# Kernel optimization log

Hardware: AMD Instinct MI355X
Metric: run time of the kernel (lower is better)

The kernel has to match this reference:

```python
import jax, jax.numpy as jnp
import numpy as np
from functools import partial

N = 8192      # nodes
E = 524288    # edges (before self-loops)
D = 64        # hidden dim (in_features == out_features)
L = 9         # conv layers: 1 start + (n_layers-2)=8 middle
MLP = 3       # depth_of_mlp


def setup_inputs() -> dict:
    key = jax.random.key(0)
    ks = jax.random.split(key, 12)
    s = 0.1  # weight scale
    return {
        "node_feat": jax.random.normal(ks[0], (N, 1), dtype=jnp.float32),
        "edge_src": jax.random.randint(ks[1], (E,), 0, N, dtype=jnp.int32),
        "edge_dst": jax.random.randint(ks[2], (E,), 0, N, dtype=jnp.int32),
        # stacked per-layer conv params (all layers operate at width D)
        "conv_W":  jax.random.normal(ks[3], (L, D, D), dtype=jnp.float32) * s,
        "conv_b":  jax.random.normal(ks[4], (L, D), dtype=jnp.float32) * s,
        "gru_Wih": jax.random.normal(ks[5], (L, 3 * D, D), dtype=jnp.float32) * s,
        "gru_Whh": jax.random.normal(ks[6], (L, 3 * D, D), dtype=jnp.float32) * s,
        "gru_bih": jax.random.normal(ks[7], (L, 3 * D), dtype=jnp.float32) * s,
        "gru_bhh": jax.random.normal(ks[8], (L, 3 * D), dtype=jnp.float32) * s,
        "mlp_W":   jax.random.normal(ks[9], (MLP, D, D), dtype=jnp.float32) * s,
        "mlp_b":   jax.random.normal(ks[10], (MLP, D), dtype=jnp.float32) * s,
    }


def _forward(node_feat, edge_src, edge_dst,
             conv_W, conv_b, gru_Wih, gru_Whh, gru_bih, gru_bhh,
             mlp_W, mlp_b):
    # dgl.add_self_loop
    loop = jnp.arange(N, dtype=edge_src.dtype)
    src = jnp.concatenate([edge_src, loop])
    dst = jnp.concatenate([edge_dst, loop])

    # GatedGraphConv pads feat with zeros up to out_feats
    h0 = jnp.pad(node_feat, ((0, 0), (0, D - node_feat.shape[1])))

    def conv_layer(h, params):
        W, b, Wih, Whh, bih, bhh = params
        hl = h @ W.T + b                                   # [N, D]
        # copy_u -> sum aggregation (gather from src, scatter-add to dst)
        a = jax.ops.segment_sum(hl[src], dst, num_segments=N)  # [N, D]
        # torch.nn.GRUCell (gate order: r, z, n)
        gi = a @ Wih.T + bih                               # [N, 3D]
        gh = h @ Whh.T + bhh                               # [N, 3D]
        i_r, i_z, i_n = jnp.split(gi, 3, axis=-1)
        h_r, h_z, h_n = jnp.split(gh, 3, axis=-1)
        r = jax.nn.sigmoid(i_r + h_r)
        z = jax.nn.sigmoid(i_z + h_z)
        n = jnp.tanh(i_n + r * h_n)
        h_new = (1.0 - z) * n + z * h
        return jax.nn.relu(h_new), None                    # F.relu after each conv

    h, _ = jax.lax.scan(conv_layer, h0,
                        (conv_W, conv_b, gru_Wih, gru_Whh, gru_bih, gru_bhh))

    # lastmlp: (Linear -> ReLU) x depth_of_mlp
    for i in range(MLP):
        h = jax.nn.relu(h @ mlp_W[i].T + mlp_b[i])

    edge_sim = h @ h.T                                     # [N, N]
    return edge_sim[None]                                  # [1, N, N]


def reference(node_feat, edge_src, edge_dst,
              conv_W, conv_b, gru_Wih, gru_Whh, gru_bih, gru_bhh,
              mlp_W, mlp_b):
    return _forward(node_feat, edge_src, edge_dst,
                    conv_W, conv_b, gru_Wih, gru_Whh, gru_bih, gru_bhh,
                    mlp_W, mlp_b)
```

## Files before the change

### kernel.cpp

```cpp
#include <hip/hip_runtime.h>
#include <math.h>

#define NNODES 8192
#define DDIM   64
#define NLAYER 9
#define NMLP   3

typedef short bfrag8 __attribute__((ext_vector_type(8)));
typedef float facc16 __attribute__((ext_vector_type(16)));

__global__ void prep_weights(const float* __restrict__ conv_W,
                             const float* __restrict__ gru_Whh,
                             const float* __restrict__ gru_Wih,
                             const float* __restrict__ mlp_W,
                             float* __restrict__ WtA,
                             float* __restrict__ WtI,
                             float* __restrict__ WtM)
{
    int tid = blockIdx.x * blockDim.x + threadIdx.x;
    const int nA = NLAYER * 64 * 256;
    const int nI = NLAYER * 64 * 192;
    const int nM = NMLP * 64 * 64;
    if (tid < nA) {
        int l = tid / 16384, rem = tid % 16384;
        int k = rem / 256, c = rem % 256;
        float v = (c < 64) ? conv_W[l * 4096 + c * 64 + k]
                           : gru_Whh[l * 12288 + (c - 64) * 64 + k];
        WtA[tid] = v;
    } else if (tid < nA + nI) {
        int t = tid - nA;
        int l = t / 12288, rem = t % 12288;
        int k = rem / 192, c = rem % 192;
        WtI[t] = gru_Wih[l * 12288 + c * 64 + k];
    } else if (tid < nA + nI + nM) {
        int t = tid - nA - nI;
        int m = t / 4096, rem = t % 4096;
        int k = rem / 64, c = rem % 64;
        WtM[t] = mlp_W[m * 4096 + c * 64 + k];
    }
}

__global__ void init_h(const float* __restrict__ node_feat,
                       float* __restrict__ h, int* __restrict__ counts)
{
    int tid = blockIdx.x * blockDim.x + threadIdx.x;
    if (tid < NNODES * DDIM) {
        int n = tid >> 6, d = tid & 63;
        h[tid] = (d == 0) ? node_feat[n] : 0.f;
    }
    if (tid < NNODES) counts[tid] = 0;
}

__global__ void count_deg(const int* __restrict__ dst, int E, int* __restrict__ counts)
{
    int tid = blockIdx.x * blockDim.x + threadIdx.x;
    if (tid < E) atomicAdd(&counts[dst[tid]], 1);
}

__global__ void scan_deg(const int* __restrict__ counts,
                         int* __restrict__ row_ptr, int* __restrict__ row_fill)
{
    __shared__ int partial[256];
    int t = threadIdx.x;
    int local[32];
    int base = t * 32;
    int s = 0;
    #pragma unroll
    for (int i = 0; i < 32; i++) { local[i] = counts[base + i]; s += local[i]; }
    partial[t] = s;
    __syncthreads();
    for (int off = 1; off < 256; off <<= 1) {
        int v = (t >= off) ? partial[t - off] : 0;
        __syncthreads();
        partial[t] += v;
        __syncthreads();
    }
    int run = (t == 0) ? 0 : partial[t - 1];
    #pragma unroll
    for (int i = 0; i < 32; i++) {
        row_ptr[base + i] = run;
        row_fill[base + i] = run;
        run += local[i];
    }
    if (t == 255) row_ptr[NNODES] = run;
}

__global__ void scatter_edges(const int* __restrict__ src, const int* __restrict__ dst, int E,
                              int* __restrict__ row_fill, int* __restrict__ col_idx)
{
    int tid = blockIdx.x * blockDim.x + threadIdx.x;
    if (tid < E) {
        int pos = atomicAdd(&row_fill[dst[tid]], 1);
        col_idx[pos] = src[tid];
    }
}

__global__ __launch_bounds__(256)
void layer_pre(const float* __restrict__ h,
               const float* __restrict__ Wt,
               const float* __restrict__ bA,
               const float* __restrict__ bH,
               float* __restrict__ hl, float* __restrict__ gh)
{
    __shared__ float ht[8][64];
    int c = threadIdx.x;
    int row0 = blockIdx.x * 8;
    ((float2*)ht)[c] = ((const float2*)(h + row0 * 64))[c];
    __syncthreads();
    float bias = (c < 64) ? bA[c] : bH[c - 64];
    float acc[8];
    #pragma unroll
    for (int r = 0; r < 8; r++) acc[r] = bias;
    #pragma unroll 8
    for (int k = 0; k < 64; k++) {
        float w = Wt[k * 256 + c];
        #pragma unroll
        for (int r = 0; r < 8; r++) acc[r] = fmaf(ht[r][k], w, acc[r]);
    }
    if (c < 64) {
        #pragma unroll
        for (int r = 0; r < 8; r++) hl[(row0 + r) * 64 + c] = acc[r];
    } else {
        int cc = c - 64;
        #pragma unroll
        for (int r = 0; r < 8; r++) gh[(row0 + r) * 192 + cc] = acc[r];
    }
}

__device__ __forceinline__ float sigmoidf_(float x) { return 1.f / (1.f + __expf(-x)); }
__device__ __forceinline__ float tanhf_(float x) {
    float e = __expf(-2.f * fabsf(x));
    float t = (1.f - e) / (1.f + e);
    return copysignf(t, x);
}

__global__ __launch_bounds__(256)
void layer_gru_agg(const float* __restrict__ hl,
                   const int* __restrict__ row_ptr,
                   const int* __restrict__ col_idx,
                   const float* __restrict__ WtI_l,
                   const float* __restrict__ bih,
                   const float* __restrict__ gh,
                   float* __restrict__ h)
{
    __shared__ float at[8][64];
    int tid = threadIdx.x;
    int d = tid & 63, rg = tid >> 6;
    int row0 = blockIdx.x * 8;
    #pragma unroll
    for (int s = 0; s < 2; s++) {
        int node = row0 + rg * 2 + s;
        int s0 = row_ptr[node], s1 = row_ptr[node + 1];
        float acc = hl[node * 64 + d];
        int e = s0;
        for (; e + 4 <= s1; e += 4) {
            int n0 = col_idx[e], n1 = col_idx[e + 1], n2 = col_idx[e + 2], n3 = col_idx[e + 3];
            float v0 = hl[n0 * 64 + d];
            float v1 = hl[n1 * 64 + d];
            float v2 = hl[n2 * 64 + d];
            float v3 = hl[n3 * 64 + d];
            acc += (v0 + v1) + (v2 + v3);
        }
        for (; e < s1; ++e)
            acc += hl[col_idx[e] * 64 + d];
        at[rg * 2 + s][d] = acc;
    }
    __syncthreads();
    float br = bih[d], bz = bih[64 + d], bn = bih[128 + d];
    float ar[2] = {br, br}, az[2] = {bz, bz}, an[2] = {bn, bn};
    #pragma unroll 8
    for (int k = 0; k < 64; k++) {
        float wr = WtI_l[k * 192 + d];
        float wz = WtI_l[k * 192 + 64 + d];
        float wn = WtI_l[k * 192 + 128 + d];
        #pragma unroll
        for (int s = 0; s < 2; s++) {
            float av = at[rg * 2 + s][k];
            ar[s] = fmaf(av, wr, ar[s]);
            az[s] = fmaf(av, wz, az[s]);
            an[s] = fmaf(av, wn, an[s]);
        }
    }
    #pragma unroll
    for (int s = 0; s < 2; s++) {
        int node = row0 + rg * 2 + s;
        float ghr = gh[node * 192 + d];
        float ghz = gh[node * 192 + 64 + d];
        float ghn = gh[node * 192 + 128 + d];
        float hv  = h[node * 64 + d];
        float r = sigmoidf_(ar[s] + ghr);
        float z = sigmoidf_(az[s] + ghz);
        float n = tanhf_(an[s] + r * ghn);
        float hn = (1.f - z) * n + z * hv;
        h[node * 64 + d] = fmaxf(hn, 0.f);
    }
}

__global__ __launch_bounds__(256)
void mlp_layer(const float* __restrict__ WtM_m,
               const float* __restrict__ b,
               float* __restrict__ h)
{
    __shared__ float ht[8][64];
    int tid = threadIdx.x;
    int d = tid & 63, rg = tid >> 6;
    int row0 = blockIdx.x * 8;
    ((float2*)ht)[tid] = ((const float2*)(h + row0 * 64))[tid];
    __syncthreads();
    float acc0 = b[d], acc1 = b[d];
    #pragma unroll 8
    for (int k = 0; k < 64; k++) {
        float w = WtM_m[k * 64 + d];
        acc0 = fmaf(ht[rg * 2 + 0][k], w, acc0);
        acc1 = fmaf(ht[rg * 2 + 1][k], w, acc1);
    }
    h[(row0 + rg * 2 + 0) * 64 + d] = fmaxf(acc0, 0.f);
    h[(row0 + rg * 2 + 1) * 64 + d] = fmaxf(acc1, 0.f);
}

__device__ __forceinline__ unsigned short f2bf_rne(float x) {
    unsigned int u = __float_as_uint(x);
    u += 0x7fffu + ((u >> 16) & 1u);
    return (unsigned short)(u >> 16);
}
__device__ __forceinline__ float bf2f(unsigned short b) {
    return __uint_as_float(((unsigned int)b) << 16);
}

__global__ __launch_bounds__(256)
void split_bf16(const float* __restrict__ h,
                unsigned short* __restrict__ h_hi,
                unsigned short* __restrict__ h_lo)
{
    int tid = blockIdx.x * blockDim.x + threadIdx.x;
    float x = h[tid];
    unsigned short hi = f2bf_rne(x);
    float r = x - bf2f(hi);
    h_hi[tid] = hi;
    h_lo[tid] = f2bf_rne(r);
}

__global__ __launch_bounds__(256)
void simmat_mfma(const unsigned short* __restrict__ h_hi,
                 const unsigned short* __restrict__ h_lo,
                 float* __restrict__ out)
{
    __shared__ uint4 smem[4096];
    int tid = threadIdx.x;
    int l = tid & 63, w = tid >> 6;
    int by = blockIdx.y, bx = blockIdx.x;

    #pragma unroll
    for (int q = 0; q < 8; q++) {
        int idx = tid + 256 * q;
        int row = idx >> 4, seg = idx & 15;
        const unsigned short* baseAB = (seg < 8) ? h_hi : h_lo;
        uint4 va = ((const uint4*)(baseAB + (by * 128 + row) * 64))[seg & 7];
        smem[row * 16 + (seg ^ (row & 15))] = va;
        uint4 vb = ((const uint4*)(baseAB + (bx * 128 + row) * 64))[seg & 7];
        smem[2048 + row * 16 + (seg ^ (row & 15))] = vb;
    }
    __syncthreads();

    int lr = l & 31, hi5 = l >> 5;
    facc16 acc[2][2];
    #pragma unroll
    for (int i = 0; i < 2; i++)
        #pragma unroll
        for (int j = 0; j < 2; j++) acc[i][j] = (facc16)(0.f);

    #pragma unroll
    for (int kk = 0; kk < 64; kk += 16) {
        int kq = (kk >> 3) + hi5;
        bfrag8 ahi[2], alo[2], bhi[2], blo[2];
        #pragma unroll
        for (int i = 0; i < 2; i++) {
            int arow = (w >> 1) * 64 + i * 32 + lr;
            ahi[i] = *(const bfrag8*)&smem[arow * 16 + (kq ^ (arow & 15))];
            alo[i] = *(const bfrag8*)&smem[arow * 16 + ((8 + kq) ^ (arow & 15))];
            int brow = (w & 1) * 64 + i * 32 + lr;
            bhi[i] = *(const bfrag8*)&smem[2048 + brow * 16 + (kq ^ (brow & 15))];
            blo[i] = *(const bfrag8*)&smem[2048 + brow * 16 + ((8 + kq) ^ (brow & 15))];
        }
        #pragma unroll
        for (int i = 0; i < 2; i++)
            #pragma unroll
            for (int j = 0; j < 2; j++) {
                acc[i][j] = __builtin_amdgcn_mfma_f32_32x32x16_bf16(ahi[i], bhi[j], acc[i][j], 0, 0, 0);
                acc[i][j] = __builtin_amdgcn_mfma_f32_32x32x16_bf16(ahi[i], blo[j], acc[i][j], 0, 0, 0);
                acc[i][j] = __builtin_amdgcn_mfma_f32_32x32x16_bf16(alo[i], bhi[j], acc[i][j], 0, 0, 0);
            }
    }

    int rbase = by * 128 + (w >> 1) * 64;
    int cbase = bx * 128 + (w & 1) * 64;
    int crow0 = rbase + 4 * hi5;
    int ccol0 = cbase + lr;
    #pragma unroll
    for (int i = 0; i < 2; i++)
        #pragma unroll
        for (int j = 0; j < 2; j++) {
            #pragma unroll
            for (int reg = 0; reg < 16; reg++) {
                int row = crow0 + i * 32 + (reg & 3) + 8 * (reg >> 2);
                int col = ccol0 + j * 32;
                out[(size_t)row * 8192 + col] = acc[i][j][reg];
            }
        }
}

extern "C" void kernel_launch(void* const* d_in, const int* in_sizes, int n_in,
                              void* d_out, int out_size, void* d_ws, size_t ws_size,
                              hipStream_t stream)
{
    const float* node_feat = (const float*)d_in[0];
    const int*   edge_src  = (const int*)d_in[1];
    const int*   edge_dst  = (const int*)d_in[2];
    const float* conv_W    = (const float*)d_in[3];
    const float* conv_b    = (const float*)d_in[4];
    const float* gru_Wih   = (const float*)d_in[5];
    const float* gru_Whh   = (const float*)d_in[6];
    const float* gru_bih   = (const float*)d_in[7];
    const float* gru_bhh   = (const float*)d_in[8];
    const float* mlp_W     = (const float*)d_in[9];
    const float* mlp_b     = (const float*)d_in[10];
    int E = in_sizes[1];
    float* out = (float*)d_out;

    float* ws  = (float*)d_ws;
    float* h   = ws;
    float* hl  = h  + NNODES * DDIM;
    float* gh  = hl + NNODES * DDIM;
    float* WtA = gh + NNODES * 192;
    float* WtI = WtA + NLAYER * 64 * 256;
    float* WtM = WtI + NLAYER * 64 * 192;
    int* counts   = (int*)(WtM + NMLP * 64 * 64);
    int* row_ptr  = counts + NNODES;
    int* row_fill = row_ptr + NNODES + 1;
    int* col_idx  = row_fill + NNODES;
    unsigned short* h_hi = (unsigned short*)((((uintptr_t)(col_idx + E)) + 15) & ~(uintptr_t)15);
    unsigned short* h_lo = h_hi + NNODES * DDIM;

    prep_weights<<<1056, 256, 0, stream>>>(conv_W, gru_Whh, gru_Wih, mlp_W, WtA, WtI, WtM);
    init_h<<<(NNODES * DDIM + 255) / 256, 256, 0, stream>>>(node_feat, h, counts);
    count_deg<<<(E + 255) / 256, 256, 0, stream>>>(edge_dst, E, counts);
    scan_deg<<<1, 256, 0, stream>>>(counts, row_ptr, row_fill);
    scatter_edges<<<(E + 255) / 256, 256, 0, stream>>>(edge_src, edge_dst, E, row_fill, col_idx);

    for (int l = 0; l < NLAYER; l++) {
        layer_pre<<<NNODES / 8, 256, 0, stream>>>(h, WtA + l * 16384,
                                                  conv_b + l * 64, gru_bhh + l * 192, hl, gh);
        layer_gru_agg<<<NNODES / 8, 256, 0, stream>>>(hl, row_ptr, col_idx,
                                                      WtI + l * 12288,
                                                      gru_bih + l * 192, gh, h);
    }
    for (int m = 0; m < NMLP; m++) {
        mlp_layer<<<NNODES / 8, 256, 0, stream>>>(WtM + m * 4096, mlp_b + m * 64, h);
    }
    split_bf16<<<NNODES * DDIM / 256, 256, 0, stream>>>(h, h_hi, h_lo);
    dim3 g(64, 64);
    simmat_mfma<<<g, 256, 0, stream>>>(h_hi, h_lo, out);
}
```

Baseline: 691.3 us.

## Aggregate raw h before conv linear and fuse each layer into one kernel

Uses linearity: the sum of (h W^T + b) over neighbours becomes (sum of h) W^T + deg*b, so the gather runs on the raw input h and the conv linear, the hidden-gate GEMM and the GRU all happen in one kernel per layer, with ping-pong h buffers. This removes the hl/gh intermediate round trips and halves the per-layer launches. It also merges the three MLP layers and the bf16 split into one kernel, and folds init/count into the weight-prep kernel with a memset. Per-block work grows (three small GEMMs per block), which may raise register pressure and lower occupancy, and the reordered summation changes floating-point rounding.

```diff
diff --git a/kernel.cpp b/kernel.cpp
--- a/kernel.cpp
+++ b/kernel.cpp
@@ -9,13 +9,17 @@
 typedef short bfrag8 __attribute__((ext_vector_type(8)));
 typedef float facc16 __attribute__((ext_vector_type(16)));
 
-__global__ void prep_weights(const float* __restrict__ conv_W,
-                             const float* __restrict__ gru_Whh,
-                             const float* __restrict__ gru_Wih,
-                             const float* __restrict__ mlp_W,
-                             float* __restrict__ WtA,
-                             float* __restrict__ WtI,
-                             float* __restrict__ WtM)
+__global__ void prep_all(const float* __restrict__ conv_W,
+                         const float* __restrict__ gru_Whh,
+                         const float* __restrict__ gru_Wih,
+                         const float* __restrict__ mlp_W,
+                         const float* __restrict__ node_feat,
+                         const int* __restrict__ edge_dst,
+                         float* __restrict__ WtA,
+                         float* __restrict__ WtI,
+                         float* __restrict__ WtM,
+                         float* __restrict__ h0,
+                         int* __restrict__ counts, int E)
 {
     int tid = blockIdx.x * blockDim.x + threadIdx.x;
     const int nA = NLAYER * 64 * 256;
@@ -24,9 +28,8 @@
     if (tid < nA) {
         int l = tid / 16384, rem = tid % 16384;
         int k = rem / 256, c = rem % 256;
-        float v = (c < 64) ? conv_W[l * 4096 + c * 64 + k]
-                           : gru_Whh[l * 12288 + (c - 64) * 64 + k];
-        WtA[tid] = v;
+        WtA[tid] = (c < 64) ? conv_W[l * 4096 + c * 64 + k]
+                            : gru_Whh[l * 12288 + (c - 64) * 64 + k];
     } else if (tid < nA + nI) {
         int t = tid - nA;
         int l = t / 12288, rem = t % 12288;
@@ -38,23 +41,11 @@
         int k = rem / 64, c = rem % 64;
         WtM[t] = mlp_W[m * 4096 + c * 64 + k];
     }
-}
-
-__global__ void init_h(const float* __restrict__ node_feat,
-                       float* __restrict__ h, int* __restrict__ counts)
-{
-    int tid = blockIdx.x * blockDim.x + threadIdx.x;
-    if (tid < NNODES * DDIM) {
+    {
         int n = tid >> 6, d = tid & 63;
-        h[tid] = (d == 0) ? node_feat[n] : 0.f;
-    }
-    if (tid < NNODES) counts[tid] = 0;
-}
-
-__global__ void count_deg(const int* __restrict__ dst, int E, int* __restrict__ counts)
-{
-    int tid = blockIdx.x * blockDim.x + threadIdx.x;
-    if (tid < E) atomicAdd(&counts[dst[tid]], 1);
+        h0[tid] = (d == 0) ? node_feat[n] : 0.f;
+    }
+    if (tid < E) atomicAdd(&counts[edge_dst[tid]], 1);
 }
 
 __global__ void scan_deg(const int* __restrict__ counts,
@@ -95,38 +86,6 @@
     }
 }
 
-__global__ __launch_bounds__(256)
-void layer_pre(const float* __restrict__ h,
-               const float* __restrict__ Wt,
-               const float* __restrict__ bA,
-               const float* __restrict__ bH,
-               float* __restrict__ hl, float* __restrict__ gh)
-{
-    __shared__ float ht[8][64];
-    int c = threadIdx.x;
-    int row0 = blockIdx.x * 8;
-    ((float2*)ht)[c] = ((const float2*)(h + row0 * 64))[c];
-    __syncthreads();
-    float bias = (c < 64) ? bA[c] : bH[c - 64];
-    float acc[8];
-    #pragma unroll
-    for (int r = 0; r < 8; r++) acc[r] = bias;
-    #pragma unroll 8
-    for (int k = 0; k < 64; k++) {
-        float w = Wt[k * 256 + c];
-        #pragma unroll
-        for (int r = 0; r < 8; r++) acc[r] = fmaf(ht[r][k], w, acc[r]);
-    }
-    if (c < 64) {
-        #pragma unroll
-        for (int r = 0; r < 8; r++) hl[(row0 + r) * 64 + c] = acc[r];
-    } else {
-        int cc = c - 64;
-        #pragma unroll
-        for (int r = 0; r < 8; r++) gh[(row0 + r) * 192 + cc] = acc[r];
-    }
-}
-
 __device__ __forceinline__ float sigmoidf_(float x) { return 1.f / (1.f + __expf(-x)); }
 __device__ __forceinline__ float tanhf_(float x) {
     float e = __expf(-2.f * fabsf(x));
@@ -135,87 +94,95 @@
 }
 
 __global__ __launch_bounds__(256)
-void layer_gru_agg(const float* __restrict__ hl,
-                   const int* __restrict__ row_ptr,
-                   const int* __restrict__ col_idx,
-                   const float* __restrict__ WtI_l,
-                   const float* __restrict__ bih,
-                   const float* __restrict__ gh,
-                   float* __restrict__ h)
-{
-    __shared__ float at[8][64];
+void layer_full(const float* __restrict__ hin,
+                const int* __restrict__ row_ptr,
+                const int* __restrict__ col_idx,
+                const float* __restrict__ WtA_l,
+                const float* __restrict__ WtI_l,
+                const float* __restrict__ cb,
+                const float* __restrict__ bih,
+                const float* __restrict__ bhh,
+                float* __restrict__ hout)
+{
+    __shared__ float hloc[8][64];
+    __shared__ float agg[8][64];
+    __shared__ float aLDS[8][64];
     int tid = threadIdx.x;
     int d = tid & 63, rg = tid >> 6;
     int row0 = blockIdx.x * 8;
+    ((float2*)hloc)[tid] = ((const float2*)(hin + row0 * 64))[tid];
     #pragma unroll
     for (int s = 0; s < 2; s++) {
         int node = row0 + rg * 2 + s;
         int s0 = row_ptr[node], s1 = row_ptr[node + 1];
-        float acc = hl[node * 64 + d];
+        float acc = hin[node * 64 + d];
         int e = s0;
         for (; e + 4 <= s1; e += 4) {
             int n0 = col_idx[e], n1 = col_idx[e + 1], n2 = col_idx[e + 2], n3 = col_idx[e + 3];
-            float v0 = hl[n0 * 64 + d];
-            float v1 = hl[n1 * 64 + d];
-            float v2 = hl[n2 * 64 + d];
-            float v3 = hl[n3 * 64 + d];
+            float v0 = hin[n0 * 64 + d];
+            float v1 = hin[n1 * 64 + d];
+            float v2 = hin[n2 * 64 + d];
+            float v3 = hin[n3 * 64 + d];
             acc += (v0 + v1) + (v2 + v3);
         }
         for (; e < s1; ++e)
-            acc += hl[col_idx[e] * 64 + d];
-        at[rg * 2 + s][d] = acc;
-    }
-    __syncthreads();
-    float br = bih[d], bz = bih[64 + d], bn = bih[128 + d];
-    float ar[2] = {br, br}, az[2] = {bz, bz}, an[2] = {bn, bn};
-    #pragma unroll 8
+            acc += hin[col_idx[e] * 64 + d];
+        agg[rg * 2 + s][d] = acc;
+    }
+    __syncthreads();
+    {
+        int r0 = rg * 2, r1 = rg * 2 + 1;
+        float deg0 = (float)(row_ptr[row0 + r0 + 1] - row_ptr[row0 + r0] + 1);
+        float deg1 = (float)(row_ptr[row0 + r1 + 1] - row_ptr[row0 + r1] + 1);
+        float cbd = cb[d];
+        float a0 = deg0 * cbd, a1 = deg1 * cbd;
+        #pragma unroll 8
+        for (int k = 0; k < 64; k++) {
+            float w = WtA_l[k * 256 + d];
+            a0 = fmaf(agg[r0][k], w, a0);
+            a1 = fmaf(agg[r1][k], w, a1);
+        }
+        aLDS[r0][d] = a0;
+        aLDS[r1][d] = a1;
+    }
+    __syncthreads();
+    float gir[2], giz[2], gin[2], ghr[2], ghz[2], ghn[2];
+    {
+        float br = bih[d], bz = bih[64 + d], bn = bih[128 + d];
+        float cr = bhh[d], cz = bhh[64 + d], cn = bhh[128 + d];
+        #pragma unroll
+        for (int s = 0; s < 2; s++) { gir[s]=br; giz[s]=bz; gin[s]=bn; ghr[s]=cr; ghz[s]=cz; ghn[s]=cn; }
+    }
+    #pragma unroll 4
     for (int k = 0; k < 64; k++) {
-        float wr = WtI_l[k * 192 + d];
-        float wz = WtI_l[k * 192 + 64 + d];
-        float wn = WtI_l[k * 192 + 128 + d];
+        float wir = WtI_l[k * 192 + d];
+        float wiz = WtI_l[k * 192 + 64 + d];
+        float win = WtI_l[k * 192 + 128 + d];
+        float whr = WtA_l[k * 256 + 64 + d];
+        float whz = WtA_l[k * 256 + 128 + d];
+        float whn = WtA_l[k * 256 + 192 + d];
         #pragma unroll
         for (int s = 0; s < 2; s++) {
-            float av = at[rg * 2 + s][k];
-            ar[s] = fmaf(av, wr, ar[s]);
-            az[s] = fmaf(av, wz, az[s]);
-            an[s] = fmaf(av, wn, an[s]);
+            float av = aLDS[rg * 2 + s][k];
+            float hv = hloc[rg * 2 + s][k];
+            gir[s] = fmaf(av, wir, gir[s]);
+            giz[s] = fmaf(av, wiz, giz[s]);
+            gin[s] = fmaf(av, win, gin[s]);
+            ghr[s] = fmaf(hv, whr, ghr[s]);
+            ghz[s] = fmaf(hv, whz, ghz[s]);
+            ghn[s] = fmaf(hv, whn, ghn[s]);
         }
     }
     #pragma unroll
     for (int s = 0; s < 2; s++) {
-        int node = row0 + rg * 2 + s;
-        float ghr = gh[node * 192 + d];
-        float ghz = gh[node * 192 + 64 + d];
-        float ghn = gh[node * 192 + 128 + d];
-        float hv  = h[node * 64 + d];
-        float r = sigmoidf_(ar[s] + ghr);
-        float z = sigmoidf_(az[s] + ghz);
-        float n = tanhf_(an[s] + r * ghn);
-        float hn = (1.f - z) * n + z * hv;
-        h[node * 64 + d] = fmaxf(hn, 0.f);
-    }
-}
-
-__global__ __launch_bounds__(256)
-void mlp_layer(const float* __restrict__ WtM_m,
-               const float* __restrict__ b,
-               float* __restrict__ h)
-{
-    __shared__ float ht[8][64];
-    int tid = threadIdx.x;
-    int d = tid & 63, rg = tid >> 6;
-    int row0 = blockIdx.x * 8;
-    ((float2*)ht)[tid] = ((const float2*)(h + row0 * 64))[tid];
-    __syncthreads();
-    float acc0 = b[d], acc1 = b[d];
-    #pragma unroll 8
-    for (int k = 0; k < 64; k++) {
-        float w = WtM_m[k * 64 + d];
-        acc0 = fmaf(ht[rg * 2 + 0][k], w, acc0);
-        acc1 = fmaf(ht[rg * 2 + 1][k], w, acc1);
-    }
-    h[(row0 + rg * 2 + 0) * 64 + d] = fmaxf(acc0, 0.f);
-    h[(row0 + rg * 2 + 1) * 64 + d] = fmaxf(acc1, 0.f);
+        int row = row0 + rg * 2 + s;
+        float r = sigmoidf_(gir[s] + ghr[s]);
+        float z = sigmoidf_(giz[s] + ghz[s]);
+        float n = tanhf_(gin[s] + r * ghn[s]);
+        float hv = hloc[rg * 2 + s][d];
+        float hnew = (1.f - z) * n + z * hv;
+        hout[row * 64 + d] = fmaxf(hnew, 0.f);
+    }
 }
 
 __device__ __forceinline__ unsigned short f2bf_rne(float x) {
@@ -228,16 +195,42 @@
 }
 
 __global__ __launch_bounds__(256)
-void split_bf16(const float* __restrict__ h,
-                unsigned short* __restrict__ h_hi,
-                unsigned short* __restrict__ h_lo)
-{
-    int tid = blockIdx.x * blockDim.x + threadIdx.x;
-    float x = h[tid];
-    unsigned short hi = f2bf_rne(x);
-    float r = x - bf2f(hi);
-    h_hi[tid] = hi;
-    h_lo[tid] = f2bf_rne(r);
+void mlp_split(const float* __restrict__ WtM,
+               const float* __restrict__ mlp_b,
+               const float* __restrict__ hin,
+               unsigned short* __restrict__ h_hi,
+               unsigned short* __restrict__ h_lo)
+{
+    __shared__ float buf0[8][64], buf1[8][64];
+    int tid = threadIdx.x, d = tid & 63, rg = tid >> 6;
+    int row0 = blockIdx.x * 8;
+    ((float2*)buf0)[tid] = ((const float2*)(hin + row0 * 64))[tid];
+    __syncthreads();
+    #pragma unroll
+    for (int m = 0; m < 3; m++) {
+        const float* Wm = WtM + m * 4096;
+        float bias = mlp_b[m * 64 + d];
+        float (*src)[64] = (m & 1) ? buf1 : buf0;
+        float (*dst)[64] = (m & 1) ? buf0 : buf1;
+        float a0 = bias, a1 = bias;
+        #pragma unroll 8
+        for (int k = 0; k < 64; k++) {
+            float w = Wm[k * 64 + d];
+            a0 = fmaf(src[rg * 2 + 0][k], w, a0);
+            a1 = fmaf(src[rg * 2 + 1][k], w, a1);
+        }
+        dst[rg * 2 + 0][d] = fmaxf(a0, 0.f);
+        dst[rg * 2 + 1][d] = fmaxf(a1, 0.f);
+        __syncthreads();
+    }
+    #pragma unroll
+    for (int s = 0; s < 2; s++) {
+        int row = row0 + rg * 2 + s;
+        float x = buf1[rg * 2 + s][d];
+        unsigned short hi = f2bf_rne(x);
+        h_hi[row * 64 + d] = hi;
+        h_lo[row * 64 + d] = f2bf_rne(x - bf2f(hi));
+    }
 }
 
 __global__ __launch_bounds__(256)
@@ -328,10 +321,9 @@
     float* out = (float*)d_out;
 
     float* ws  = (float*)d_ws;
-    float* h   = ws;
-    float* hl  = h  + NNODES * DDIM;
-    float* gh  = hl + NNODES * DDIM;
-    float* WtA = gh + NNODES * 192;
+    float* h0  = ws;
+    float* h1  = h0 + NNODES * DDIM;
+    float* WtA = h1 + NNODES * DDIM;
     float* WtI = WtA + NLAYER * 64 * 256;
     float* WtM = WtI + NLAYER * 64 * 192;
     int* counts   = (int*)(WtM + NMLP * 64 * 64);
@@ -341,23 +333,24 @@
     unsigned short* h_hi = (unsigned short*)((((uintptr_t)(col_idx + E)) + 15) & ~(uintptr_t)15);
     unsigned short* h_lo = h_hi + NNODES * DDIM;
 
-    prep_weights<<<1056, 256, 0, stream>>>(conv_W, gru_Whh, gru_Wih, mlp_W, WtA, WtI, WtM);
-    init_h<<<(NNODES * DDIM + 255) / 256, 256, 0, stream>>>(node_feat, h, counts);
-    count_deg<<<(E + 255) / 256, 256, 0, stream>>>(edge_dst, E, counts);
+    hipMemsetAsync(counts, 0, NNODES * sizeof(int), stream);
+    prep_all<<<2048, 256, 0, stream>>>(conv_W, gru_Whh, gru_Wih, mlp_W,
+                                       node_feat, edge_dst,
+                                       WtA, WtI, WtM, h0, counts, E);
     scan_deg<<<1, 256, 0, stream>>>(counts, row_ptr, row_fill);
     scatter_edges<<<(E + 255) / 256, 256, 0, stream>>>(edge_src, edge_dst, E, row_fill, col_idx);
 
+    const float* cur = h0;
+    float* nxt = h1;
     for (int l = 0; l < NLAYER; l++) {
-        layer_pre<<<NNODES / 8, 256, 0, stream>>>(h, WtA + l * 16384,
-                                                  conv_b + l * 64, gru_bhh + l * 192, hl, gh);
-        layer_gru_agg<<<NNODES / 8, 256, 0, stream>>>(hl, row_ptr, col_idx,
-                                                      WtI + l * 12288,
-                                                      gru_bih + l * 192, gh, h);
-    }
-    for (int m = 0; m < NMLP; m++) {
-        mlp_layer<<<NNODES / 8, 256, 0, stream>>>(WtM + m * 4096, mlp_b + m * 64, h);
-    }
-    split_bf16<<<NNODES * DDIM / 256, 256, 0, stream>>>(h, h_hi, h_lo);
+        layer_full<<<NNODES / 8, 256, 0, stream>>>(cur, row_ptr, col_idx,
+                                                   WtA + l * 16384, WtI + l * 12288,
+                                                   conv_b + l * 64,
+                                                   gru_bih + l * 192, gru_bhh + l * 192,
+                                                   nxt);
+        const float* t = cur; cur = nxt; nxt = (float*)t;
+    }
+    mlp_split<<<NNODES / 8, 256, 0, stream>>>(WtM, mlp_b, cur, h_hi, h_lo);
     dim3 g(64, 64);
     simmat_mfma<<<g, 256, 0, stream>>>(h_hi, h_lo, out);
 }
```

Result: no change. 678.4 us (-1.9%).
